# Kernel optimization log

Measured on AMD Instinct MI355X. Metric: run time of the kernel, lower is better.

Reference implementation:

```python
import jax, jax.numpy as jnp
import numpy as np

N = 100000
SK = [10, 5]
LN_EPS = 1e-5


def setup_inputs() -> dict:
    key = jax.random.key(0)
    ks = jax.random.split(key, 12)
    F_IN, H, OUT = 256, 128, 64
    X = jax.random.normal(ks[0], (N, F_IN), dtype=jnp.float32)
    edge_index = jax.random.randint(ks[1], (2, 1600000), 0, N, dtype=jnp.int64)
    # cached sampled-neighbor index lists: cumulative fanout 10, then 10*5=50 per node
    sn0 = jax.random.randint(ks[2], (N * SK[0],), 0, N, dtype=jnp.int64)
    sn1 = jax.random.randint(ks[3], (N * SK[0] * SK[1],), 0, N, dtype=jnp.int64)
    s1 = 1.0 / np.sqrt(F_IN)
    s2 = 1.0 / np.sqrt(2 * H)
    s3 = 1.0 / np.sqrt(H)
    W1 = jax.random.uniform(ks[4], (F_IN, H), jnp.float32, -s1, s1)
    b1 = jax.random.uniform(ks[5], (H,), jnp.float32, -s1, s1)
    W2 = jax.random.uniform(ks[6], (2 * H, H), jnp.float32, -s2, s2)
    b2 = jax.random.uniform(ks[7], (H,), jnp.float32, -s2, s2)
    gamma = jnp.ones((H,), jnp.float32)
    beta = jnp.zeros((H,), jnp.float32)
    W3 = jax.random.uniform(ks[8], (H, OUT), jnp.float32, -s3, s3)
    b3 = jax.random.uniform(ks[9], (OUT,), jnp.float32, -s3, s3)
    return {"X": X, "edge_index": edge_index, "sn0": sn0, "sn1": sn1,
            "W1": W1, "b1": b1, "W2": W2, "b2": b2,
            "gamma": gamma, "beta": beta, "W3": W3, "b3": b3}


def _layernorm(x, gamma, beta):
    mu = jnp.mean(x, axis=-1, keepdims=True)
    var = jnp.mean(jnp.square(x - mu), axis=-1, keepdims=True)
    return (x - mu) * jax.lax.rsqrt(var + LN_EPS) * gamma + beta


def reference(X, edge_index, sn0, sn1, W1, b1, W2, b2, gamma, beta, W3, b3):
    # edge_index is only used in the original to build the cached adjacency
    # used for sampling; sampled indices (sn0, sn1) are precomputed inputs.
    del edge_index
    h = X @ W1 + b1  # [N, H]
    num_update = 1
    for sn, k in ((sn0, SK[0]), (sn1, SK[1])):
        num_update *= k
        # neighbor gather + sum reduce: [N*num_update, H] -> [N, num_update, H] -> [N, H]
        agg = h[sn].reshape(N, num_update, -1).sum(axis=1)
        h = jnp.concatenate([h, agg], axis=1) @ W2 + b2  # concat agg_hidden
        h = _layernorm(jax.nn.relu(h), gamma, beta)
    return h @ W3 + b3
```

## Files before the change

### kernel.cpp

```cpp
#include <hip/hip_runtime.h>


typedef unsigned short u16;
typedef unsigned int   u32;

#define NN  100000
#define NT  6250
#define HID 128
#define FIN 256

typedef __attribute__((ext_vector_type(8))) short bf16x8;
typedef __attribute__((ext_vector_type(4))) float f32x4;

__device__ __forceinline__ u16 f2bf(float f) {
  u32 x = __builtin_bit_cast(u32, f);
  x += 0x7fffu + ((x >> 16) & 1u);
  return (u16)(x >> 16);
}
__device__ __forceinline__ float bflo(u32 v) { return __builtin_bit_cast(float, v << 16); }
__device__ __forceinline__ float bfhi(u32 v) { return __builtin_bit_cast(float, v & 0xffff0000u); }

__global__ __launch_bounds__(256) void prep_kernel(
    const float* __restrict__ W1, const float* __restrict__ W2, const float* __restrict__ W3,
    u16* __restrict__ W1T, u16* __restrict__ W2T, u16* __restrict__ W3T) {
  int t = blockIdx.x * 256 + threadIdx.x;
  if (t < FIN * HID) {
    int k = t >> 7, c = t & (HID - 1);
    W1T[c * FIN + k] = f2bf(W1[t]);
    W2T[c * FIN + k] = f2bf(W2[t]);
  }
  if (t < HID * 64) {
    int k = t >> 6, c = t & 63;
    W3T[c * HID + k] = f2bf(W3[t]);
  }
}

__global__ __launch_bounds__(256) void proj_kernel(
    const float* __restrict__ X, const float* __restrict__ b1,
    const u16* __restrict__ W1T, u16* __restrict__ h1) {
  const int w = threadIdx.x >> 6, l = threadIdx.x & 63;
  const int tile = blockIdx.x * 4 + w;
  if (tile >= NT) return;
  const int lr = l & 15, lg = l >> 4;

  bf16x8 a[8];
  const float* xb = X + (tile * 16 + lr) * FIN + lg * 8;
  #pragma unroll
  for (int s = 0; s < 8; ++s) {
    const float4* p = (const float4*)(xb + s * 32);
    float4 x0 = p[0], x1 = p[1];
    bf16x8 t;
    t[0] = (short)f2bf(x0.x); t[1] = (short)f2bf(x0.y);
    t[2] = (short)f2bf(x0.z); t[3] = (short)f2bf(x0.w);
    t[4] = (short)f2bf(x1.x); t[5] = (short)f2bf(x1.y);
    t[6] = (short)f2bf(x1.z); t[7] = (short)f2bf(x1.w);
    a[s] = t;
  }
  #pragma unroll
  for (int n = 0; n < 8; ++n) {
    const int col = n * 16 + lr;
    f32x4 c = {0.f, 0.f, 0.f, 0.f};
    const bf16x8* wp = (const bf16x8*)(W1T + col * FIN + lg * 8);
    #pragma unroll
    for (int s = 0; s < 8; ++s)
      c = __builtin_amdgcn_mfma_f32_16x16x32_bf16(a[s], wp[s * 4], c, 0, 0, 0);
    const float bias = b1[col];
    #pragma unroll
    for (int r = 0; r < 4; ++r)
      h1[(tile * 16 + lg * 4 + r) * HID + col] = f2bf(c[r] + bias);
  }
}

template <int KN, bool FINAL>
__global__ __launch_bounds__(512, 4) void layer_kernel(
    const u16* __restrict__ hin, const int* __restrict__ sn,
    const u16* __restrict__ W2T, const float* __restrict__ b2,
    const float* __restrict__ gamma, const float* __restrict__ beta,
    const u16* __restrict__ W3T, const float* __restrict__ b3,
    u16* __restrict__ hout, float* __restrict__ out) {
  __shared__ u16 At[8][16][264];
  const int w = threadIdx.x >> 6, l = threadIdx.x & 63;
  const int lr = l & 15, lg = l >> 4;
  const int tile = blockIdx.x * 8 + w;
  const bool active = tile < NT;

  if (active) {
    const u16* hp = hin + 2 * l;
    for (int n = 0; n < 16; ++n) {
      const int node = __builtin_amdgcn_readfirstlane(tile * 16 + n);
      const u32 sv = *(const u32*)(hp + node * HID);
      *(u32*)&At[w][n][2 * l] = sv;
      float a0 = 0.f, a1 = 0.f;
      #pragma unroll 10
      for (int j = 0; j < KN; ++j) {
        const int idx = sn[node * KN + j];
        const u32 v = *(const u32*)(hp + idx * HID);
        a0 += bflo(v); a1 += bfhi(v);
      }
      *(u32*)&At[w][n][HID + 2 * l] = ((u32)f2bf(a1) << 16) | (u32)f2bf(a0);
    }
  }
  __syncthreads();

  f32x4 acc[8];
  if (active) {
    bf16x8 a[8];
    #pragma unroll
    for (int s = 0; s < 8; ++s)
      a[s] = *(const bf16x8*)&At[w][lr][s * 32 + lg * 8];
    #pragma unroll
    for (int n = 0; n < 8; ++n) {
      f32x4 c = {0.f, 0.f, 0.f, 0.f};
      const bf16x8* wp = (const bf16x8*)(W2T + (n * 16 + lr) * FIN + lg * 8);
      #pragma unroll
      for (int s = 0; s < 8; ++s)
        c = __builtin_amdgcn_mfma_f32_16x16x32_bf16(a[s], wp[s * 4], c, 0, 0, 0);
      acc[n] = c;
    }
    #pragma unroll
    for (int n = 0; n < 8; ++n) {
      const float bias = b2[n * 16 + lr];
      #pragma unroll
      for (int r = 0; r < 4; ++r) {
        const float v = acc[n][r] + bias;
        acc[n][r] = v > 0.f ? v : 0.f;
      }
    }
    #pragma unroll
    for (int r = 0; r < 4; ++r) {
      float s1 = 0.f, s2 = 0.f;
      #pragma unroll
      for (int n = 0; n < 8; ++n) { const float v = acc[n][r]; s1 += v; s2 += v * v; }
      s1 += __shfl_xor(s1, 1); s2 += __shfl_xor(s2, 1);
      s1 += __shfl_xor(s1, 2); s2 += __shfl_xor(s2, 2);
      s1 += __shfl_xor(s1, 4); s2 += __shfl_xor(s2, 4);
      s1 += __shfl_xor(s1, 8); s2 += __shfl_xor(s2, 8);
      const float mu  = s1 * (1.f / 128.f);
      const float var = s2 * (1.f / 128.f) - mu * mu;
      const float rstd = rsqrtf(var + 1e-5f);
      #pragma unroll
      for (int n = 0; n < 8; ++n)
        acc[n][r] = (acc[n][r] - mu) * rstd;
    }
  }

  if constexpr (!FINAL) {
    if (active) {
      #pragma unroll
      for (int n = 0; n < 8; ++n) {
        const int col = n * 16 + lr;
        const float g = gamma[col], bb = beta[col];
        #pragma unroll
        for (int r = 0; r < 4; ++r)
          hout[(tile * 16 + lg * 4 + r) * HID + col] = f2bf(acc[n][r] * g + bb);
      }
    }
  } else {
    if (active) {
      #pragma unroll
      for (int n = 0; n < 8; ++n) {
        const int col = n * 16 + lr;
        const float g = gamma[col], bb = beta[col];
        #pragma unroll
        for (int r = 0; r < 4; ++r)
          At[w][lg * 4 + r][col] = f2bf(acc[n][r] * g + bb);
      }
    }
    __syncthreads();
    if (active) {
      bf16x8 a2[4];
      #pragma unroll
      for (int s = 0; s < 4; ++s)
        a2[s] = *(const bf16x8*)&At[w][lr][s * 32 + lg * 8];
      #pragma unroll
      for (int n = 0; n < 4; ++n) {
        f32x4 c = {0.f, 0.f, 0.f, 0.f};
        const bf16x8* wp = (const bf16x8*)(W3T + (n * 16 + lr) * HID + lg * 8);
        #pragma unroll
        for (int s = 0; s < 4; ++s)
          c = __builtin_amdgcn_mfma_f32_16x16x32_bf16(a2[s], wp[s * 4], c, 0, 0, 0);
        const int col = n * 16 + lr;
        const float bias = b3[col];
        #pragma unroll
        for (int r = 0; r < 4; ++r)
          out[(tile * 16 + lg * 4 + r) * 64 + col] = c[r] + bias;
      }
    }
  }
}

extern "C" void kernel_launch(void* const* d_in, const int* in_sizes, int n_in,
                              void* d_out, int out_size, void* d_ws, size_t ws_size,
                              hipStream_t stream) {
  (void)in_sizes; (void)n_in; (void)out_size; (void)ws_size;
  const float* X   = (const float*)d_in[0];
  const int*   sn0 = (const int*)d_in[2];
  const int*   sn1 = (const int*)d_in[3];
  const float* W1  = (const float*)d_in[4];
  const float* b1  = (const float*)d_in[5];
  const float* W2  = (const float*)d_in[6];
  const float* b2  = (const float*)d_in[7];
  const float* gm  = (const float*)d_in[8];
  const float* bt  = (const float*)d_in[9];
  const float* W3  = (const float*)d_in[10];
  const float* b3  = (const float*)d_in[11];
  float* out = (float*)d_out;

  char* ws = (char*)d_ws;
  u16* h1  = (u16*)(ws);
  u16* h2  = (u16*)(ws + 25600000);
  u16* W1T = (u16*)(ws + 51200000);
  u16* W2T = (u16*)(ws + 51265536);
  u16* W3T = (u16*)(ws + 51331072);

  prep_kernel<<<128, 256, 0, stream>>>(W1, W2, W3, W1T, W2T, W3T);
  proj_kernel<<<(NT + 3) / 4, 256, 0, stream>>>(X, b1, W1T, h1);
  layer_kernel<10, false><<<(NT + 7) / 8, 512, 0, stream>>>(
      h1, sn0, W2T, b2, gm, bt, nullptr, nullptr, h2, nullptr);
  layer_kernel<50, true><<<(NT + 7) / 8, 512, 0, stream>>>(
      h2, sn1, W2T, b2, gm, bt, W3T, b3, nullptr, out);
}
```

Baseline: 585.9 us.

## Split neighbor gather into a standalone one-wave-per-node kernel

Moves the neighbor gather-sum out of the fused layer kernel into a separate gather kernel. Each wave now handles one node, with the neighbor loop fully unrolled, so many more independent loads are in flight. The MLP kernel then loads self and aggregated rows straight from global memory, and LDS is used only in the final layer. In exchange, each layer writes and re-reads an extra aggregate buffer. Workspace slots are reused by aliasing, which relies on each wave reading its own rows before writing them.

```diff
diff --git a/kernel.cpp b/kernel.cpp
--- a/kernel.cpp
+++ b/kernel.cpp
@@ -71,43 +71,48 @@
   }
 }
 
-template <int KN, bool FINAL>
-__global__ __launch_bounds__(512, 4) void layer_kernel(
-    const u16* __restrict__ hin, const int* __restrict__ sn,
+template <int KN>
+__global__ __launch_bounds__(256, 6) void gather_kernel(
+    const u16* __restrict__ h, const int* __restrict__ sn, u16* __restrict__ agg) {
+  const int wid = (int)((blockIdx.x * 256u + threadIdx.x) >> 6);
+  if (wid >= NN) return;
+  const int node = __builtin_amdgcn_readfirstlane(wid);
+  const int l = threadIdx.x & 63;
+  const u16* hp = h + 2 * l;
+  const int* sp = sn + (size_t)node * KN;
+  float a0 = 0.f, a1 = 0.f;
+  #pragma unroll
+  for (int j = 0; j < KN; ++j) {
+    const int idx = sp[j];
+    const u32 v = *(const u32*)(hp + (size_t)idx * HID);
+    a0 += bflo(v); a1 += bfhi(v);
+  }
+  *(u32*)(agg + (size_t)node * HID + 2 * l) = ((u32)f2bf(a1) << 16) | (u32)f2bf(a0);
+}
+
+template <bool FINAL>
+__global__ __launch_bounds__(512, 4) void mlp_kernel(
+    const u16* __restrict__ hin, const u16* __restrict__ aggin,
     const u16* __restrict__ W2T, const float* __restrict__ b2,
     const float* __restrict__ gamma, const float* __restrict__ beta,
     const u16* __restrict__ W3T, const float* __restrict__ b3,
     u16* __restrict__ hout, float* __restrict__ out) {
-  __shared__ u16 At[8][16][264];
   const int w = threadIdx.x >> 6, l = threadIdx.x & 63;
   const int lr = l & 15, lg = l >> 4;
   const int tile = blockIdx.x * 8 + w;
   const bool active = tile < NT;
 
-  if (active) {
-    const u16* hp = hin + 2 * l;
-    for (int n = 0; n < 16; ++n) {
-      const int node = __builtin_amdgcn_readfirstlane(tile * 16 + n);
-      const u32 sv = *(const u32*)(hp + node * HID);
-      *(u32*)&At[w][n][2 * l] = sv;
-      float a0 = 0.f, a1 = 0.f;
-      #pragma unroll 10
-      for (int j = 0; j < KN; ++j) {
-        const int idx = sn[node * KN + j];
-        const u32 v = *(const u32*)(hp + idx * HID);
-        a0 += bflo(v); a1 += bfhi(v);
-      }
-      *(u32*)&At[w][n][HID + 2 * l] = ((u32)f2bf(a1) << 16) | (u32)f2bf(a0);
-    }
-  }
-  __syncthreads();
-
   f32x4 acc[8];
   if (active) {
+    const int row = tile * 16 + lr;
     bf16x8 a[8];
-    #pragma unroll
-    for (int s = 0; s < 8; ++s)
-      a[s] = *(const bf16x8*)&At[w][lr][s * 32 + lg * 8];
+    const u16* hb = hin  + (size_t)row * HID + lg * 8;
+    const u16* ab = aggin + (size_t)row * HID + lg * 8;
+    #pragma unroll
+    for (int s = 0; s < 4; ++s) a[s]     = *(const bf16x8*)(hb + s * 32);
+    #pragma unroll
+    for (int s = 0; s < 4; ++s) a[4 + s] = *(const bf16x8*)(ab + s * 32);
+
     #pragma unroll
     for (int n = 0; n < 8; ++n) {
       f32x4 c = {0.f, 0.f, 0.f, 0.f};
@@ -152,10 +157,11 @@
         const float g = gamma[col], bb = beta[col];
         #pragma unroll
         for (int r = 0; r < 4; ++r)
-          hout[(tile * 16 + lg * 4 + r) * HID + col] = f2bf(acc[n][r] * g + bb);
+          hout[(size_t)(tile * 16 + lg * 4 + r) * HID + col] = f2bf(acc[n][r] * g + bb);
       }
     }
   } else {
+    __shared__ u16 At[8][16][264];
     if (active) {
       #pragma unroll
       for (int n = 0; n < 8; ++n) {
@@ -183,7 +189,7 @@
         const float bias = b3[col];
         #pragma unroll
         for (int r = 0; r < 4; ++r)
-          out[(tile * 16 + lg * 4 + r) * 64 + col] = c[r] + bias;
+          out[(size_t)(tile * 16 + lg * 4 + r) * 64 + col] = c[r] + bias;
       }
     }
   }
@@ -207,16 +213,23 @@
   float* out = (float*)d_out;
 
   char* ws = (char*)d_ws;
-  u16* h1  = (u16*)(ws);
-  u16* h2  = (u16*)(ws + 25600000);
+  u16* slotA = (u16*)(ws);
+  u16* slotB = (u16*)(ws + 25600000);
   u16* W1T = (u16*)(ws + 51200000);
   u16* W2T = (u16*)(ws + 51265536);
   u16* W3T = (u16*)(ws + 51331072);
 
+  u16* h1 = slotA;
+  u16* agg1 = slotB;
+  u16* h2 = slotB;
+  u16* agg2 = slotA;
+
   prep_kernel<<<128, 256, 0, stream>>>(W1, W2, W3, W1T, W2T, W3T);
   proj_kernel<<<(NT + 3) / 4, 256, 0, stream>>>(X, b1, W1T, h1);
-  layer_kernel<10, false><<<(NT + 7) / 8, 512, 0, stream>>>(
-      h1, sn0, W2T, b2, gm, bt, nullptr, nullptr, h2, nullptr);
-  layer_kernel<50, true><<<(NT + 7) / 8, 512, 0, stream>>>(
-      h2, sn1, W2T, b2, gm, bt, W3T, b3, nullptr, out);
-}
+  gather_kernel<10><<<NN / 4, 256, 0, stream>>>(h1, sn0, agg1);
+  mlp_kernel<false><<<(NT + 7) / 8, 512, 0, stream>>>(
+      h1, agg1, W2T, b2, gm, bt, nullptr, nullptr, h2, nullptr);
+  gather_kernel<50><<<NN / 4, 256, 0, stream>>>(h2, sn1, agg2);
+  mlp_kernel<true><<<(NT + 7) / 8, 512, 0, stream>>>(
+      h2, agg2, W2T, b2, gm, bt, W3T, b3, nullptr, out);
+}
```

Result: no change. 577.7 us (-1.4%).
